# Optimization experiments

Hardware: AMD Instinct MI355X
Metric: run time of the kernel (lower is better)

The kernel has to match this reference:

```python
import jax, jax.numpy as jnp
import numpy as np

B, T, V, E, H = 16, 64, 32000, 256, 1024
NEG = -1e9


def lstm_step(kernel, bias, x, h, c):
    # TF BasicLSTMCell: gates ordered i, j, f, o; forget_bias = 1.0
    z = jnp.concatenate([x, h], axis=-1) @ kernel + bias
    i, j, f, o = jnp.split(z, 4, axis=-1)
    c_new = c * jax.nn.sigmoid(f + 1.0) + jax.nn.sigmoid(i) * jnp.tanh(j)
    h_new = jnp.tanh(c_new) * jax.nn.sigmoid(o)
    return h_new, c_new


def setup_inputs() -> dict:
    key = jax.random.key(0)
    ks = jax.random.split(key, 14)
    s = 0.05
    return {
        "encoder_inputs": jax.random.randint(ks[0], (B, T), 0, V, dtype=jnp.int32),
        "decoder_inputs": jax.random.randint(ks[1], (B, T), 0, V, dtype=jnp.int32),
        "encoder_lengths": jax.random.randint(ks[2], (B,), 1, T + 1, dtype=jnp.int32),
        "decoder_lengths": jax.random.randint(ks[3], (B,), 1, T + 1, dtype=jnp.int32),
        "embedding": jax.random.uniform(ks[4], (V, E), jnp.float32, -1 / 16, 1 / 16),
        "enc_kernel": jax.random.normal(ks[5], (E + H, 4 * H), jnp.float32) * s,
        "enc_bias": jnp.zeros((4 * H,), jnp.float32),
        "dec_kernel": jax.random.normal(ks[6], (E + H + H, 4 * H), jnp.float32) * s,
        "dec_bias": jnp.zeros((4 * H,), jnp.float32),
        "Wm": jax.random.normal(ks[7], (H, H), jnp.float32) * s,
        "Wq": jax.random.normal(ks[8], (H, H), jnp.float32) * s,
        "v_att": jax.random.normal(ks[9], (H,), jnp.float32) * s,
        "attn_kernel": jax.random.normal(ks[10], (2 * H, H), jnp.float32) * s,
        "out_kernel": jax.random.normal(ks[11], (H, V), jnp.float32) * s,
    }


def _forward(encoder_inputs, decoder_inputs, encoder_lengths, decoder_lengths,
             embedding, enc_kernel, enc_bias, dec_kernel, dec_bias,
             Wm, Wq, v_att, attn_kernel, out_kernel):
    q_emb = embedding[encoder_inputs]  # [B,T,E]
    r_emb = embedding[decoder_inputs]  # [B,T,E]

    # ---- encoder: dynamic_rnn with sequence_length semantics ----
    def enc_step(carry, inp):
        h, c = carry
        x, t = inp
        h2, c2 = lstm_step(enc_kernel, enc_bias, x, h, c)
        valid = (t < encoder_lengths)[:, None]
        h = jnp.where(valid, h2, h)
        c = jnp.where(valid, c2, c)
        out = jnp.where(valid, h2, 0.0)
        return (h, c), out

    h0 = jnp.zeros((B, H), jnp.float32)
    (enc_h, enc_c), memory_tm = jax.lax.scan(
        enc_step, (h0, h0), (q_emb.transpose(1, 0, 2), jnp.arange(T)))
    memory = memory_tm.transpose(1, 0, 2)  # [B,T,H]

    keys = memory @ Wm  # precomputed Bahdanau memory projection [B,T,H]
    score_mask = jnp.arange(T)[None, :] < encoder_lengths[:, None]  # [B,T]

    # ---- decoder: AttentionWrapper(BasicLSTMCell) + TrainingHelper ----
    def dec_step(carry, inp):
        h, c, attn = carry
        x_emb, t = inp
        x = jnp.concatenate([x_emb, attn], axis=-1)  # [B, E+H]
        h2, c2 = lstm_step(dec_kernel, dec_bias, x, h, c)
        query = h2 @ Wq  # [B,H]
        scores = jnp.einsum('bth,h->bt', jnp.tanh(keys + query[:, None, :]), v_att)
        scores = jnp.where(score_mask, scores, NEG)
        align = jax.nn.softmax(scores, axis=-1)  # [B,T]
        context = jnp.einsum('bt,bth->bh', align, memory)
        attn2 = jnp.concatenate([h2, context], axis=-1) @ attn_kernel  # [B,H]
        finished = (t >= decoder_lengths)[:, None]
        out = jnp.where(finished, 0.0, attn2)  # dynamic_decode zeros finished
        return (h2, c2, attn2), out

    attn0 = jnp.zeros((B, H), jnp.float32)
    _, dec_tm = jax.lax.scan(
        dec_step, (enc_h, enc_c, attn0), (r_emb.transpose(1, 0, 2), jnp.arange(T)))
    dec_out = dec_tm.transpose(1, 0, 2)  # [B,T,H]

    logits = jnp.einsum('bth,hv->btv', dec_out, out_kernel)  # [B,T,V]
    return logits


def reference(encoder_inputs, decoder_inputs, encoder_lengths, decoder_lengths,
              embedding, enc_kernel, enc_bias, dec_kernel, dec_bias,
              Wm, Wq, v_att, attn_kernel, out_kernel):
    return _forward(encoder_inputs, decoder_inputs, encoder_lengths, decoder_lengths,
                    embedding, enc_kernel, enc_bias, dec_kernel, dec_bias,
                    Wm, Wq, v_att, attn_kernel, out_kernel)
```

## Files before the change

### kernel.cpp

```cpp
#include <hip/hip_runtime.h>
#include <hip/hip_bf16.h>

#define B_ 16
#define T_ 64
#define V_ 32000
#define E_ 256
#define H_ 1024
#define G4_ (4 * H_)
#define KE_ (E_ + H_)
#define KD_ (E_ + 2*H_)
#define NKS_ 32
#define KSE_ (KE_ / NKS_)
#define KSD_ (KD_ / NKS_)

typedef unsigned short ushort_t;
typedef unsigned int uint_t;

__device__ __forceinline__ float b2f(ushort_t u) {
    return __uint_as_float(((uint_t)u) << 16);
}
__device__ __forceinline__ ushort_t f2b(float f) {
    uint_t u = __float_as_uint(f);
    u = (u + 0x7fffu + ((u >> 16) & 1u)) >> 16;
    return (ushort_t)u;
}
__device__ __forceinline__ float sigf(float x) {
    return 1.f / (1.f + expf(-x));
}

__global__ __launch_bounds__(256) void init_kernel(float* __restrict__ p, int n)
{
    int i = blockIdx.x * 256 + threadIdx.x;
    if (i < n) p[i] = 0.f;
}

__global__ __launch_bounds__(256) void enc_gemm_kernel(
    const float* __restrict__ emb, const int* __restrict__ enc_in,
    const float* __restrict__ Wk, const float* __restrict__ h_in,
    float* __restrict__ zpart, int t)
{
    const int cc = blockIdx.x & 15;
    const int ks = blockIdx.x >> 4;
    const int col = cc * 256 + threadIdx.x;
    const int k0 = ks * KSE_;

    int vidx[16];
    #pragma unroll
    for (int b = 0; b < 16; ++b) vidx[b] = enc_in[b * T_ + t];

    float acc[16];
    #pragma unroll
    for (int b = 0; b < 16; ++b) acc[b] = 0.f;

    for (int kk = 0; kk < KSE_; ++kk) {
        const int k = k0 + kk;
        const float w = Wk[(size_t)k * G4_ + col];
        if (k < E_) {
            #pragma unroll
            for (int b = 0; b < 16; ++b)
                acc[b] = fmaf(emb[(size_t)vidx[b] * E_ + k], w, acc[b]);
        } else {
            const float* hp = h_in + (k - E_);
            #pragma unroll
            for (int b = 0; b < 16; ++b)
                acc[b] = fmaf(hp[b * H_], w, acc[b]);
        }
    }
    #pragma unroll
    for (int b = 0; b < 16; ++b)
        zpart[((size_t)(ks * 16 + b)) * G4_ + col] = acc[b];
}

__global__ __launch_bounds__(256) void enc_gates_kernel(
    const float* __restrict__ zpart, const float* __restrict__ bias,
    const int* __restrict__ enc_len, const float* __restrict__ h_in,
    float* __restrict__ h_out, float* __restrict__ c,
    float* __restrict__ memory, int t)
{
    const int idx = blockIdx.x * 256 + threadIdx.x;
    const int b = idx >> 10, hu = idx & 1023;
    float z[4];
    #pragma unroll
    for (int g = 0; g < 4; ++g) {
        float s0 = bias[g * H_ + hu], s1 = 0.f, s2 = 0.f, s3 = 0.f;
        #pragma unroll
        for (int ks = 0; ks < NKS_; ks += 4) {
            s0 += zpart[((size_t)((ks + 0) * 16 + b)) * G4_ + g * H_ + hu];
            s1 += zpart[((size_t)((ks + 1) * 16 + b)) * G4_ + g * H_ + hu];
            s2 += zpart[((size_t)((ks + 2) * 16 + b)) * G4_ + g * H_ + hu];
            s3 += zpart[((size_t)((ks + 3) * 16 + b)) * G4_ + g * H_ + hu];
        }
        z[g] = (s0 + s1) + (s2 + s3);
    }
    const float cold = c[b * H_ + hu];
    const float cn = cold * sigf(z[2] + 1.f) + sigf(z[0]) * tanhf(z[1]);
    const float hn = tanhf(cn) * sigf(z[3]);
    const bool valid = t < enc_len[b];
    h_out[b * H_ + hu] = valid ? hn : h_in[b * H_ + hu];
    c[b * H_ + hu]     = valid ? cn : cold;
    memory[((size_t)b * T_ + t) * H_ + hu] = valid ? hn : 0.f;
}

__global__ __launch_bounds__(256) void keys_gemm_kernel(
    const float* __restrict__ memory, const float* __restrict__ Wm,
    float* __restrict__ keys)
{
    const int rt = blockIdx.x >> 2;
    const int cc = blockIdx.x & 3;
    const int col = cc * 256 + threadIdx.x;
    float acc[16];
    #pragma unroll
    for (int m = 0; m < 16; ++m) acc[m] = 0.f;
    for (int k = 0; k < H_; ++k) {
        const float w = Wm[(size_t)k * H_ + col];
        const float* mp = memory + (size_t)(rt * 16) * H_ + k;
        #pragma unroll
        for (int m = 0; m < 16; ++m)
            acc[m] = fmaf(mp[(size_t)m * H_], w, acc[m]);
    }
    #pragma unroll
    for (int m = 0; m < 16; ++m)
        keys[(size_t)(rt * 16 + m) * H_ + col] = acc[m];
}

__global__ __launch_bounds__(256) void dec_gemm_kernel(
    const float* __restrict__ emb, const int* __restrict__ dec_in,
    const float* __restrict__ Wk, const float* __restrict__ attn,
    const float* __restrict__ h_in, float* __restrict__ zpart, int t)
{
    const int cc = blockIdx.x & 15;
    const int ks = blockIdx.x >> 4;
    const int col = cc * 256 + threadIdx.x;
    const int k0 = ks * KSD_;

    int vidx[16];
    #pragma unroll
    for (int b = 0; b < 16; ++b) vidx[b] = dec_in[b * T_ + t];

    float acc[16];
    #pragma unroll
    for (int b = 0; b < 16; ++b) acc[b] = 0.f;

    for (int kk = 0; kk < KSD_; ++kk) {
        const int k = k0 + kk;
        const float w = Wk[(size_t)k * G4_ + col];
        if (k < E_) {
            #pragma unroll
            for (int b = 0; b < 16; ++b)
                acc[b] = fmaf(emb[(size_t)vidx[b] * E_ + k], w, acc[b]);
        } else if (k < E_ + H_) {
            const float* ap = attn + (k - E_);
            #pragma unroll
            for (int b = 0; b < 16; ++b)
                acc[b] = fmaf(ap[b * H_], w, acc[b]);
        } else {
            const float* hp = h_in + (k - E_ - H_);
            #pragma unroll
            for (int b = 0; b < 16; ++b)
                acc[b] = fmaf(hp[b * H_], w, acc[b]);
        }
    }
    #pragma unroll
    for (int b = 0; b < 16; ++b)
        zpart[((size_t)(ks * 16 + b)) * G4_ + col] = acc[b];
}

__global__ __launch_bounds__(256) void dec_gates_kernel(
    const float* __restrict__ zpart, const float* __restrict__ bias,
    float* __restrict__ h_out, float* __restrict__ c)
{
    const int idx = blockIdx.x * 256 + threadIdx.x;
    const int b = idx >> 10, hu = idx & 1023;
    float z[4];
    #pragma unroll
    for (int g = 0; g < 4; ++g) {
        float s0 = bias[g * H_ + hu], s1 = 0.f, s2 = 0.f, s3 = 0.f;
        #pragma unroll
        for (int ks = 0; ks < NKS_; ks += 4) {
            s0 += zpart[((size_t)((ks + 0) * 16 + b)) * G4_ + g * H_ + hu];
            s1 += zpart[((size_t)((ks + 1) * 16 + b)) * G4_ + g * H_ + hu];
            s2 += zpart[((size_t)((ks + 2) * 16 + b)) * G4_ + g * H_ + hu];
            s3 += zpart[((size_t)((ks + 3) * 16 + b)) * G4_ + g * H_ + hu];
        }
        z[g] = (s0 + s1) + (s2 + s3);
    }
    const float cold = c[b * H_ + hu];
    const float cn = cold * sigf(z[2] + 1.f) + sigf(z[0]) * tanhf(z[1]);
    const float hn = tanhf(cn) * sigf(z[3]);
    h_out[b * H_ + hu] = hn;
    c[b * H_ + hu] = cn;
}

__global__ __launch_bounds__(256) void query_gemm_kernel(
    const float* __restrict__ h2, const float* __restrict__ Wq,
    float* __restrict__ qpart)
{
    const int cc = blockIdx.x & 3;
    const int ks = blockIdx.x >> 2;
    const int col = cc * 256 + threadIdx.x;
    const int k0 = ks * 32;
    float acc[16];
    #pragma unroll
    for (int b = 0; b < 16; ++b) acc[b] = 0.f;
    for (int kk = 0; kk < 32; ++kk) {
        const int k = k0 + kk;
        const float w = Wq[(size_t)k * H_ + col];
        const float* hp = h2 + k;
        #pragma unroll
        for (int b = 0; b < 16; ++b)
            acc[b] = fmaf(hp[b * H_], w, acc[b]);
    }
    #pragma unroll
    for (int b = 0; b < 16; ++b)
        qpart[((size_t)(ks * 16 + b)) * H_ + col] = acc[b];
}

__global__ __launch_bounds__(256) void query_finish_kernel(
    const float* __restrict__ qpart, float* __restrict__ q)
{
    const int idx = blockIdx.x * 256 + threadIdx.x;
    const int b = idx >> 10, col = idx & 1023;
    float s0 = 0.f, s1 = 0.f, s2 = 0.f, s3 = 0.f;
    #pragma unroll
    for (int ks = 0; ks < 32; ks += 4) {
        s0 += qpart[((size_t)((ks + 0) * 16 + b)) * H_ + col];
        s1 += qpart[((size_t)((ks + 1) * 16 + b)) * H_ + col];
        s2 += qpart[((size_t)((ks + 2) * 16 + b)) * H_ + col];
        s3 += qpart[((size_t)((ks + 3) * 16 + b)) * H_ + col];
    }
    q[idx] = (s0 + s1) + (s2 + s3);
}

__global__ __launch_bounds__(256) void attn_scores_kernel(
    const float* __restrict__ q, const float* __restrict__ keys,
    const float* __restrict__ v_att, float* __restrict__ scores)
{
    const int b = blockIdx.x >> 6, t = blockIdx.x & 63;
    const int tid = threadIdx.x;
    const float* kp = keys + ((size_t)b * T_ + t) * H_;
    const float* qp = q + b * H_;
    float s = 0.f;
    #pragma unroll
    for (int i = 0; i < 4; ++i) {
        const int h = tid + i * 256;
        s += tanhf(kp[h] + qp[h]) * v_att[h];
    }
    #pragma unroll
    for (int off = 32; off; off >>= 1) s += __shfl_xor(s, off);
    __shared__ float red[4];
    if ((tid & 63) == 0) red[tid >> 6] = s;
    __syncthreads();
    if (tid == 0) scores[b * T_ + t] = (red[0] + red[1]) + (red[2] + red[3]);
}

__global__ __launch_bounds__(256) void softmax_ctx_kernel(
    const float* __restrict__ scores, const float* __restrict__ memory,
    const int* __restrict__ enc_len, float* __restrict__ ctx)
{
    const int b = blockIdx.x >> 2, cc = blockIdx.x & 3;
    const int tid = threadIdx.x;
    __shared__ float al[T_];
    if (tid < 64) {
        const int len = enc_len[b];
        float s = (tid < len) ? scores[b * T_ + tid] : -1e9f;
        float m = s;
        #pragma unroll
        for (int off = 32; off; off >>= 1) m = fmaxf(m, __shfl_xor(m, off));
        float e = expf(s - m);
        float sum = e;
        #pragma unroll
        for (int off = 32; off; off >>= 1) sum += __shfl_xor(sum, off);
        al[tid] = e / sum;
    }
    __syncthreads();
    const int col = cc * 256 + tid;
    const float* mp = memory + (size_t)b * T_ * H_ + col;
    float a0 = 0.f, a1 = 0.f, a2 = 0.f, a3 = 0.f;
    #pragma unroll
    for (int t2 = 0; t2 < T_; t2 += 4) {
        a0 = fmaf(al[t2 + 0], mp[(size_t)(t2 + 0) * H_], a0);
        a1 = fmaf(al[t2 + 1], mp[(size_t)(t2 + 1) * H_], a1);
        a2 = fmaf(al[t2 + 2], mp[(size_t)(t2 + 2) * H_], a2);
        a3 = fmaf(al[t2 + 3], mp[(size_t)(t2 + 3) * H_], a3);
    }
    ctx[b * H_ + col] = (a0 + a1) + (a2 + a3);
}

__global__ __launch_bounds__(256) void attnout_gemm_kernel(
    const float* __restrict__ h2, const float* __restrict__ ctx,
    const float* __restrict__ attn_k, float* __restrict__ apart)
{
    const int cc = blockIdx.x & 3;
    const int ks = blockIdx.x >> 2;
    const int col = cc * 256 + threadIdx.x;
    const int k0 = ks * 64;
    float acc[16];
    #pragma unroll
    for (int b = 0; b < 16; ++b) acc[b] = 0.f;
    for (int kk = 0; kk < 64; ++kk) {
        const int k = k0 + kk;
        const float w = attn_k[(size_t)k * H_ + col];
        const float* xp = (k < H_) ? (h2 + k) : (ctx + (k - H_));
        #pragma unroll
        for (int b = 0; b < 16; ++b)
            acc[b] = fmaf(xp[b * H_], w, acc[b]);
    }
    #pragma unroll
    for (int b = 0; b < 16; ++b)
        apart[((size_t)(ks * 16 + b)) * H_ + col] = acc[b];
}

__global__ __launch_bounds__(256) void attnout_finish_kernel(
    const float* __restrict__ apart, const int* __restrict__ dec_len,
    float* __restrict__ attn_state, float* __restrict__ dec_out, int t)
{
    const int idx = blockIdx.x * 256 + threadIdx.x;
    const int b = idx >> 10, col = idx & 1023;
    float s0 = 0.f, s1 = 0.f, s2 = 0.f, s3 = 0.f;
    #pragma unroll
    for (int ks = 0; ks < 32; ks += 4) {
        s0 += apart[((size_t)((ks + 0) * 16 + b)) * H_ + col];
        s1 += apart[((size_t)((ks + 1) * 16 + b)) * H_ + col];
        s2 += apart[((size_t)((ks + 2) * 16 + b)) * H_ + col];
        s3 += apart[((size_t)((ks + 3) * 16 + b)) * H_ + col];
    }
    const float s = (s0 + s1) + (s2 + s3);
    attn_state[b * H_ + col] = s;
    const bool fin = t >= dec_len[b];
    dec_out[((size_t)b * T_ + t) * H_ + col] = fin ? 0.f : s;
}

typedef __attribute__((ext_vector_type(8))) short short8;
typedef __attribute__((ext_vector_type(4))) float float4v;

__global__ __launch_bounds__(256) void logits_kernel(
    const float* __restrict__ A, const float* __restrict__ Bw,
    float* __restrict__ out)
{
    __shared__ __align__(16) ushort_t Ah[64][40];
    __shared__ __align__(16) ushort_t Al[64][40];
    __shared__ __align__(16) ushort_t Bh[64][40];
    __shared__ __align__(16) ushort_t Bl[64][40];
    const int tid = threadIdx.x;
    const int m0 = blockIdx.x * 64;
    const int n0 = blockIdx.y * 64;
    const int wv = tid >> 6, lane = tid & 63;
    const int ml = lane & 15, quad = lane >> 4;

    float4v acc[4];
    #pragma unroll
    for (int nn = 0; nn < 4; ++nn) acc[nn] = (float4v){0.f, 0.f, 0.f, 0.f};

    for (int kb = 0; kb < 1024; kb += 32) {
        __syncthreads();
        {
            const int r = tid >> 2, c0 = (tid & 3) * 8;
            const float* ap = A + (size_t)(m0 + r) * 1024 + kb + c0;
            #pragma unroll
            for (int i = 0; i < 8; ++i) {
                const float f = ap[i];
                const ushort_t hi = f2b(f);
                Ah[r][c0 + i] = hi;
                Al[r][c0 + i] = f2b(f - b2f(hi));
            }
        }
        {
            const int cB = tid & 63, kq = tid >> 6;
            #pragma unroll
            for (int i = 0; i < 8; ++i) {
                const int k = kq * 8 + i;
                const float f = Bw[(size_t)(kb + k) * V_ + n0 + cB];
                const ushort_t hi = f2b(f);
                Bh[cB][k] = hi;
                Bl[cB][k] = f2b(f - b2f(hi));
            }
        }
        __syncthreads();
        const short8 afh = *(const short8*)&Ah[wv * 16 + ml][quad * 8];
        const short8 afl = *(const short8*)&Al[wv * 16 + ml][quad * 8];
        #pragma unroll
        for (int nn = 0; nn < 4; ++nn) {
            const short8 bfh = *(const short8*)&Bh[nn * 16 + ml][quad * 8];
            const short8 bfl = *(const short8*)&Bl[nn * 16 + ml][quad * 8];
            acc[nn] = __builtin_amdgcn_mfma_f32_16x16x32_bf16(afh, bfh, acc[nn], 0, 0, 0);
            acc[nn] = __builtin_amdgcn_mfma_f32_16x16x32_bf16(afh, bfl, acc[nn], 0, 0, 0);
            acc[nn] = __builtin_amdgcn_mfma_f32_16x16x32_bf16(afl, bfh, acc[nn], 0, 0, 0);
        }
    }
    #pragma unroll
    for (int nn = 0; nn < 4; ++nn) {
        #pragma unroll
        for (int rg = 0; rg < 4; ++rg) {
            const int row = m0 + wv * 16 + quad * 4 + rg;
            const int colo = n0 + nn * 16 + ml;
            out[(size_t)row * V_ + colo] = acc[nn][rg];
        }
    }
}

extern "C" void kernel_launch(void* const* d_in, const int* in_sizes, int n_in,
                              void* d_out, int out_size, void* d_ws, size_t ws_size,
                              hipStream_t stream) {
    (void)in_sizes; (void)n_in; (void)out_size; (void)ws_size;
    const int*   enc_in  = (const int*)d_in[0];
    const int*   dec_in  = (const int*)d_in[1];
    const int*   enc_len = (const int*)d_in[2];
    const int*   dec_len = (const int*)d_in[3];
    const float* emb     = (const float*)d_in[4];
    const float* encK    = (const float*)d_in[5];
    const float* encB    = (const float*)d_in[6];
    const float* decK    = (const float*)d_in[7];
    const float* decB    = (const float*)d_in[8];
    const float* Wm      = (const float*)d_in[9];
    const float* Wq      = (const float*)d_in[10];
    const float* v_att   = (const float*)d_in[11];
    const float* attnK   = (const float*)d_in[12];
    const float* outK    = (const float*)d_in[13];
    float* out = (float*)d_out;

    float* hbuf    = (float*)d_ws;
    float* cbuf    = hbuf + 2 * B_ * H_;
    float* attn    = cbuf + B_ * H_;
    float* ctx     = attn + B_ * H_;
    float* q       = ctx + B_ * H_;
    float* scores  = q + B_ * H_;
    float* memory  = scores + B_ * T_;
    float* keys    = memory + (size_t)B_ * T_ * H_;
    float* dec_out = keys + (size_t)B_ * T_ * H_;
    float* zpart   = dec_out + (size_t)B_ * T_ * H_;
    float* qpart   = zpart;
    float* apart   = zpart + (size_t)32 * B_ * H_;

    const int ninit = 4 * B_ * H_;
    init_kernel<<<(ninit + 255) / 256, 256, 0, stream>>>((float*)d_ws, ninit);

    for (int t = 0; t < T_; ++t) {
        float* h_in  = hbuf + (t & 1) * B_ * H_;
        float* h_out = hbuf + ((t + 1) & 1) * B_ * H_;
        enc_gemm_kernel<<<512, 256, 0, stream>>>(emb, enc_in, encK, h_in, zpart, t);
        enc_gates_kernel<<<64, 256, 0, stream>>>(zpart, encB, enc_len, h_in,
                                                 h_out, cbuf, memory, t);
    }
    keys_gemm_kernel<<<256, 256, 0, stream>>>(memory, Wm, keys);

    for (int t = 0; t < T_; ++t) {
        float* h_in  = hbuf + (t & 1) * B_ * H_;
        float* h2    = hbuf + ((t + 1) & 1) * B_ * H_;
        dec_gemm_kernel<<<512, 256, 0, stream>>>(emb, dec_in, decK, attn, h_in, zpart, t);
        dec_gates_kernel<<<64, 256, 0, stream>>>(zpart, decB, h2, cbuf);
        query_gemm_kernel<<<128, 256, 0, stream>>>(h2, Wq, qpart);
        query_finish_kernel<<<64, 256, 0, stream>>>(qpart, q);
        attn_scores_kernel<<<1024, 256, 0, stream>>>(q, keys, v_att, scores);
        softmax_ctx_kernel<<<64, 256, 0, stream>>>(scores, memory, enc_len, ctx);
        attnout_gemm_kernel<<<128, 256, 0, stream>>>(h2, ctx, attnK, apart);
        attnout_finish_kernel<<<64, 256, 0, stream>>>(apart, dec_len, attn, dec_out, t);
    }

    logits_kernel<<<dim3(16, 500), 256, 0, stream>>>(dec_out, outK, out);
}
```

Before: 7.006 ms.

## Fuse per-step LSTM and attention kernels using atomic grid barriers

Merges each encoder and decoder step's GEMM and gate kernels into one launch. The partial sums are reduced by the last blocks after an atomic counter barrier. The six attention-stage kernels are collapsed into one persistent kernel of 256 blocks with five grid-wide barriers, and the inner loops load inputs as float4 with weights unrolled by four rows. This removes a large number of small kernel launches per timestep, but it depends on all blocks being co-resident and adds spin-wait and threadfence overhead.

```diff
diff --git a/kernel.cpp b/kernel.cpp
--- a/kernel.cpp
+++ b/kernel.cpp
@@ -1,5 +1,4 @@
 #include <hip/hip_runtime.h>
-#include <hip/hip_bf16.h>
 
 #define B_ 16
 #define T_ 64
@@ -28,20 +27,44 @@
     return 1.f / (1.f + expf(-x));
 }
 
-__global__ __launch_bounds__(256) void init_kernel(float* __restrict__ p, int n)
+__device__ __forceinline__ void block_arrive(int* cnt) {
+    __threadfence();
+    __syncthreads();
+    if (threadIdx.x == 0)
+        __hip_atomic_fetch_add(cnt, 1, __ATOMIC_RELEASE, __HIP_MEMORY_SCOPE_AGENT);
+}
+__device__ __forceinline__ void block_wait(int* cnt, int target) {
+    if (threadIdx.x == 0) {
+        while (__hip_atomic_load(cnt, __ATOMIC_ACQUIRE, __HIP_MEMORY_SCOPE_AGENT) < target)
+            __builtin_amdgcn_s_sleep(2);
+    }
+    __syncthreads();
+}
+__device__ __forceinline__ void grid_barrier(int* cnt, int target) {
+    block_arrive(cnt);
+    block_wait(cnt, target);
+}
+
+__global__ __launch_bounds__(256) void init_kernel(float* __restrict__ state,
+                                                   int* __restrict__ cnts)
 {
-    int i = blockIdx.x * 256 + threadIdx.x;
-    if (i < n) p[i] = 0.f;
-}
-
-__global__ __launch_bounds__(256) void enc_gemm_kernel(
+    const int i = blockIdx.x * 256 + threadIdx.x;
+    if (i < 4 * B_ * H_) state[i] = 0.f;
+    if (i < 256) cnts[i] = 0;
+}
+
+__global__ __launch_bounds__(256, 2) void enc_step_kernel(
     const float* __restrict__ emb, const int* __restrict__ enc_in,
-    const float* __restrict__ Wk, const float* __restrict__ h_in,
-    float* __restrict__ zpart, int t)
+    const float* __restrict__ Wk, const float* __restrict__ bias,
+    const int* __restrict__ enc_len, const float* __restrict__ h_in,
+    float* __restrict__ h_out, float* __restrict__ c,
+    float* __restrict__ memory, float* __restrict__ zpart,
+    int* __restrict__ cnt, int t)
 {
+    const int tid = threadIdx.x;
     const int cc = blockIdx.x & 15;
     const int ks = blockIdx.x >> 4;
-    const int col = cc * 256 + threadIdx.x;
+    const int col = cc * 256 + tid;
     const int k0 = ks * KSE_;
 
     int vidx[16];
@@ -52,43 +75,55 @@
     #pragma unroll
     for (int b = 0; b < 16; ++b) acc[b] = 0.f;
 
-    for (int kk = 0; kk < KSE_; ++kk) {
-        const int k = k0 + kk;
-        const float w = Wk[(size_t)k * G4_ + col];
+    for (int g = 0; g < KSE_ / 4; ++g) {
+        const int k = k0 + g * 4;
+        const float* wp = Wk + (size_t)k * G4_ + col;
+        const float w0 = wp[0];
+        const float w1 = wp[G4_];
+        const float w2 = wp[2 * G4_];
+        const float w3 = wp[3 * G4_];
         if (k < E_) {
             #pragma unroll
-            for (int b = 0; b < 16; ++b)
-                acc[b] = fmaf(emb[(size_t)vidx[b] * E_ + k], w, acc[b]);
+            for (int b = 0; b < 16; ++b) {
+                const float4 xv = *(const float4*)(emb + (size_t)vidx[b] * E_ + k);
+                acc[b] = fmaf(xv.x, w0, acc[b]);
+                acc[b] = fmaf(xv.y, w1, acc[b]);
+                acc[b] = fmaf(xv.z, w2, acc[b]);
+                acc[b] = fmaf(xv.w, w3, acc[b]);
+            }
         } else {
             const float* hp = h_in + (k - E_);
             #pragma unroll
-            for (int b = 0; b < 16; ++b)
-                acc[b] = fmaf(hp[b * H_], w, acc[b]);
+            for (int b = 0; b < 16; ++b) {
+                const float4 xv = *(const float4*)(hp + b * H_);
+                acc[b] = fmaf(xv.x, w0, acc[b]);
+                acc[b] = fmaf(xv.y, w1, acc[b]);
+                acc[b] = fmaf(xv.z, w2, acc[b]);
+                acc[b] = fmaf(xv.w, w3, acc[b]);
+            }
         }
     }
     #pragma unroll
     for (int b = 0; b < 16; ++b)
-        zpart[((size_t)(ks * 16 + b)) * G4_ + col] = acc[b];
-}
-
-__global__ __launch_bounds__(256) void enc_gates_kernel(
-    const float* __restrict__ zpart, const float* __restrict__ bias,
-    const int* __restrict__ enc_len, const float* __restrict__ h_in,
-    float* __restrict__ h_out, float* __restrict__ c,
-    float* __restrict__ memory, int t)
-{
-    const int idx = blockIdx.x * 256 + threadIdx.x;
+        zpart[(size_t)(ks * 16 + b) * G4_ + col] = acc[b];
+
+    block_arrive(cnt);
+    if (ks < 28) return;
+    block_wait(cnt, 512);
+
+    const int tb = (ks - 28) * 16 + cc;
+    const int idx = tb * 256 + tid;
     const int b = idx >> 10, hu = idx & 1023;
     float z[4];
     #pragma unroll
     for (int g = 0; g < 4; ++g) {
         float s0 = bias[g * H_ + hu], s1 = 0.f, s2 = 0.f, s3 = 0.f;
         #pragma unroll
-        for (int ks = 0; ks < NKS_; ks += 4) {
-            s0 += zpart[((size_t)((ks + 0) * 16 + b)) * G4_ + g * H_ + hu];
-            s1 += zpart[((size_t)((ks + 1) * 16 + b)) * G4_ + g * H_ + hu];
-            s2 += zpart[((size_t)((ks + 2) * 16 + b)) * G4_ + g * H_ + hu];
-            s3 += zpart[((size_t)((ks + 3) * 16 + b)) * G4_ + g * H_ + hu];
+        for (int kss = 0; kss < NKS_; kss += 4) {
+            s0 += zpart[(size_t)((kss + 0) * 16 + b) * G4_ + g * H_ + hu];
+            s1 += zpart[(size_t)((kss + 1) * 16 + b) * G4_ + g * H_ + hu];
+            s2 += zpart[(size_t)((kss + 2) * 16 + b) * G4_ + g * H_ + hu];
+            s3 += zpart[(size_t)((kss + 3) * 16 + b) * G4_ + g * H_ + hu];
         }
         z[g] = (s0 + s1) + (s2 + s3);
     }
@@ -111,26 +146,36 @@
     float acc[16];
     #pragma unroll
     for (int m = 0; m < 16; ++m) acc[m] = 0.f;
-    for (int k = 0; k < H_; ++k) {
-        const float w = Wm[(size_t)k * H_ + col];
+    for (int g = 0; g < H_ / 4; ++g) {
+        const int k = g * 4;
+        const float* wp = Wm + (size_t)k * H_ + col;
+        const float w0 = wp[0], w1 = wp[H_], w2 = wp[2 * H_], w3 = wp[3 * H_];
         const float* mp = memory + (size_t)(rt * 16) * H_ + k;
         #pragma unroll
-        for (int m = 0; m < 16; ++m)
-            acc[m] = fmaf(mp[(size_t)m * H_], w, acc[m]);
+        for (int m = 0; m < 16; ++m) {
+            const float4 xv = *(const float4*)(mp + (size_t)m * H_);
+            acc[m] = fmaf(xv.x, w0, acc[m]);
+            acc[m] = fmaf(xv.y, w1, acc[m]);
+            acc[m] = fmaf(xv.z, w2, acc[m]);
+            acc[m] = fmaf(xv.w, w3, acc[m]);
+        }
     }
     #pragma unroll
     for (int m = 0; m < 16; ++m)
         keys[(size_t)(rt * 16 + m) * H_ + col] = acc[m];
 }
 
-__global__ __launch_bounds__(256) void dec_gemm_kernel(
+__global__ __launch_bounds__(256, 2) void dec_step_kernel(
     const float* __restrict__ emb, const int* __restrict__ dec_in,
-    const float* __restrict__ Wk, const float* __restrict__ attn,
-    const float* __restrict__ h_in, float* __restrict__ zpart, int t)
+    const float* __restrict__ Wk, const float* __restrict__ bias,
+    const float* __restrict__ attn, const float* __restrict__ h_in,
+    float* __restrict__ h_out, float* __restrict__ c,
+    float* __restrict__ zpart, int* __restrict__ cnt, int t)
 {
+    const int tid = threadIdx.x;
     const int cc = blockIdx.x & 15;
     const int ks = blockIdx.x >> 4;
-    const int col = cc * 256 + threadIdx.x;
+    const int col = cc * 256 + tid;
     const int k0 = ks * KSD_;
 
     int vidx[16];
@@ -141,46 +186,56 @@
     #pragma unroll
     for (int b = 0; b < 16; ++b) acc[b] = 0.f;
 
-    for (int kk = 0; kk < KSD_; ++kk) {
-        const int k = k0 + kk;
-        const float w = Wk[(size_t)k * G4_ + col];
+    for (int g = 0; g < KSD_ / 4; ++g) {
+        const int k = k0 + g * 4;
+        const float* wp = Wk + (size_t)k * G4_ + col;
+        const float w0 = wp[0];
+        const float w1 = wp[G4_];
+        const float w2 = wp[2 * G4_];
+        const float w3 = wp[3 * G4_];
         if (k < E_) {
             #pragma unroll
-            for (int b = 0; b < 16; ++b)
-                acc[b] = fmaf(emb[(size_t)vidx[b] * E_ + k], w, acc[b]);
-        } else if (k < E_ + H_) {
-            const float* ap = attn + (k - E_);
-            #pragma unroll
-            for (int b = 0; b < 16; ++b)
-                acc[b] = fmaf(ap[b * H_], w, acc[b]);
+            for (int b = 0; b < 16; ++b) {
+                const float4 xv = *(const float4*)(emb + (size_t)vidx[b] * E_ + k);
+                acc[b] = fmaf(xv.x, w0, acc[b]);
+                acc[b] = fmaf(xv.y, w1, acc[b]);
+                acc[b] = fmaf(xv.z, w2, acc[b]);
+                acc[b] = fmaf(xv.w, w3, acc[b]);
+            }
         } else {
-            const float* hp = h_in + (k - E_ - H_);
-            #pragma unroll
-            for (int b = 0; b < 16; ++b)
-                acc[b] = fmaf(hp[b * H_], w, acc[b]);
+            const float* xb = (k < E_ + H_) ? (attn + (k - E_))
+                                            : (h_in + (k - E_ - H_));
+            #pragma unroll
+            for (int b = 0; b < 16; ++b) {
+                const float4 xv = *(const float4*)(xb + b * H_);
+                acc[b] = fmaf(xv.x, w0, acc[b]);
+                acc[b] = fmaf(xv.y, w1, acc[b]);
+                acc[b] = fmaf(xv.z, w2, acc[b]);
+                acc[b] = fmaf(xv.w, w3, acc[b]);
+            }
         }
     }
     #pragma unroll
     for (int b = 0; b < 16; ++b)
-        zpart[((size_t)(ks * 16 + b)) * G4_ + col] = acc[b];
-}
-
-__global__ __launch_bounds__(256) void dec_gates_kernel(
-    const float* __restrict__ zpart, const float* __restrict__ bias,
-    float* __restrict__ h_out, float* __restrict__ c)
-{
-    const int idx = blockIdx.x * 256 + threadIdx.x;
+        zpart[(size_t)(ks * 16 + b) * G4_ + col] = acc[b];
+
+    block_arrive(cnt);
+    if (ks < 28) return;
+    block_wait(cnt, 512);
+
+    const int tb = (ks - 28) * 16 + cc;
+    const int idx = tb * 256 + tid;
     const int b = idx >> 10, hu = idx & 1023;
     float z[4];
     #pragma unroll
     for (int g = 0; g < 4; ++g) {
         float s0 = bias[g * H_ + hu], s1 = 0.f, s2 = 0.f, s3 = 0.f;
         #pragma unroll
-        for (int ks = 0; ks < NKS_; ks += 4) {
-            s0 += zpart[((size_t)((ks + 0) * 16 + b)) * G4_ + g * H_ + hu];
-            s1 += zpart[((size_t)((ks + 1) * 16 + b)) * G4_ + g * H_ + hu];
-            s2 += zpart[((size_t)((ks + 2) * 16 + b)) * G4_ + g * H_ + hu];
-            s3 += zpart[((size_t)((ks + 3) * 16 + b)) * G4_ + g * H_ + hu];
+        for (int kss = 0; kss < NKS_; kss += 4) {
+            s0 += zpart[(size_t)((kss + 0) * 16 + b) * G4_ + g * H_ + hu];
+            s1 += zpart[(size_t)((kss + 1) * 16 + b) * G4_ + g * H_ + hu];
+            s2 += zpart[(size_t)((kss + 2) * 16 + b) * G4_ + g * H_ + hu];
+            s3 += zpart[(size_t)((kss + 3) * 16 + b) * G4_ + g * H_ + hu];
         }
         z[g] = (s0 + s1) + (s2 + s3);
     }
@@ -191,143 +246,156 @@
     c[b * H_ + hu] = cn;
 }
 
-__global__ __launch_bounds__(256) void query_gemm_kernel(
+__global__ __launch_bounds__(256, 2) void attn_mega_kernel(
     const float* __restrict__ h2, const float* __restrict__ Wq,
-    float* __restrict__ qpart)
+    float* __restrict__ qpart, float* __restrict__ q,
+    const float* __restrict__ keys, const float* __restrict__ v_att,
+    float* __restrict__ scores, const float* __restrict__ memory,
+    const int* __restrict__ enc_len, float* __restrict__ ctx,
+    const float* __restrict__ attnK, float* __restrict__ apart,
+    const int* __restrict__ dec_len, float* __restrict__ attn_state,
+    float* __restrict__ dec_out, int* __restrict__ cnt, int t)
 {
-    const int cc = blockIdx.x & 3;
-    const int ks = blockIdx.x >> 2;
-    const int col = cc * 256 + threadIdx.x;
-    const int k0 = ks * 32;
-    float acc[16];
-    #pragma unroll
-    for (int b = 0; b < 16; ++b) acc[b] = 0.f;
-    for (int kk = 0; kk < 32; ++kk) {
-        const int k = k0 + kk;
-        const float w = Wq[(size_t)k * H_ + col];
-        const float* hp = h2 + k;
+    const int tid = threadIdx.x;
+    const int blk = blockIdx.x;
+    __shared__ float al[T_];
+    __shared__ float red[4];
+
+    {
+        const int cc = blk & 3, ks = blk >> 2;
+        const int col = cc * 256 + tid;
+        const int k0 = ks * 16;
+        float acc[16];
+        #pragma unroll
+        for (int b = 0; b < 16; ++b) acc[b] = 0.f;
+        #pragma unroll
+        for (int g = 0; g < 4; ++g) {
+            const int k = k0 + g * 4;
+            const float* wp = Wq + (size_t)k * H_ + col;
+            const float w0 = wp[0], w1 = wp[H_], w2 = wp[2 * H_], w3 = wp[3 * H_];
+            #pragma unroll
+            for (int b = 0; b < 16; ++b) {
+                const float4 xv = *(const float4*)(h2 + b * H_ + k);
+                acc[b] = fmaf(xv.x, w0, acc[b]);
+                acc[b] = fmaf(xv.y, w1, acc[b]);
+                acc[b] = fmaf(xv.z, w2, acc[b]);
+                acc[b] = fmaf(xv.w, w3, acc[b]);
+            }
+        }
         #pragma unroll
         for (int b = 0; b < 16; ++b)
-            acc[b] = fmaf(hp[b * H_], w, acc[b]);
-    }
-    #pragma unroll
-    for (int b = 0; b < 16; ++b)
-        qpart[((size_t)(ks * 16 + b)) * H_ + col] = acc[b];
-}
-
-__global__ __launch_bounds__(256) void query_finish_kernel(
-    const float* __restrict__ qpart, float* __restrict__ q)
-{
-    const int idx = blockIdx.x * 256 + threadIdx.x;
-    const int b = idx >> 10, col = idx & 1023;
-    float s0 = 0.f, s1 = 0.f, s2 = 0.f, s3 = 0.f;
-    #pragma unroll
-    for (int ks = 0; ks < 32; ks += 4) {
-        s0 += qpart[((size_t)((ks + 0) * 16 + b)) * H_ + col];
-        s1 += qpart[((size_t)((ks + 1) * 16 + b)) * H_ + col];
-        s2 += qpart[((size_t)((ks + 2) * 16 + b)) * H_ + col];
-        s3 += qpart[((size_t)((ks + 3) * 16 + b)) * H_ + col];
-    }
-    q[idx] = (s0 + s1) + (s2 + s3);
-}
-
-__global__ __launch_bounds__(256) void attn_scores_kernel(
-    const float* __restrict__ q, const float* __restrict__ keys,
-    const float* __restrict__ v_att, float* __restrict__ scores)
-{
-    const int b = blockIdx.x >> 6, t = blockIdx.x & 63;
-    const int tid = threadIdx.x;
-    const float* kp = keys + ((size_t)b * T_ + t) * H_;
-    const float* qp = q + b * H_;
-    float s = 0.f;
+            qpart[(size_t)(ks * 16 + b) * H_ + col] = acc[b];
+    }
+    grid_barrier(cnt, 256);
+
+    if (blk < 64) {
+        const int idx = blk * 256 + tid;
+        const int b = idx >> 10, col = idx & 1023;
+        float s0 = 0.f, s1 = 0.f, s2 = 0.f, s3 = 0.f;
+        #pragma unroll
+        for (int ks = 0; ks < 64; ks += 4) {
+            s0 += qpart[(size_t)((ks + 0) * 16 + b) * H_ + col];
+            s1 += qpart[(size_t)((ks + 1) * 16 + b) * H_ + col];
+            s2 += qpart[(size_t)((ks + 2) * 16 + b) * H_ + col];
+            s3 += qpart[(size_t)((ks + 3) * 16 + b) * H_ + col];
+        }
+        q[idx] = (s0 + s1) + (s2 + s3);
+    }
+    grid_barrier(cnt, 512);
+
     #pragma unroll
     for (int i = 0; i < 4; ++i) {
-        const int h = tid + i * 256;
-        s += tanhf(kp[h] + qp[h]) * v_att[h];
-    }
-    #pragma unroll
-    for (int off = 32; off; off >>= 1) s += __shfl_xor(s, off);
-    __shared__ float red[4];
-    if ((tid & 63) == 0) red[tid >> 6] = s;
-    __syncthreads();
-    if (tid == 0) scores[b * T_ + t] = (red[0] + red[1]) + (red[2] + red[3]);
-}
-
-__global__ __launch_bounds__(256) void softmax_ctx_kernel(
-    const float* __restrict__ scores, const float* __restrict__ memory,
-    const int* __restrict__ enc_len, float* __restrict__ ctx)
-{
-    const int b = blockIdx.x >> 2, cc = blockIdx.x & 3;
-    const int tid = threadIdx.x;
-    __shared__ float al[T_];
-    if (tid < 64) {
-        const int len = enc_len[b];
-        float s = (tid < len) ? scores[b * T_ + tid] : -1e9f;
-        float m = s;
-        #pragma unroll
-        for (int off = 32; off; off >>= 1) m = fmaxf(m, __shfl_xor(m, off));
-        float e = expf(s - m);
-        float sum = e;
-        #pragma unroll
-        for (int off = 32; off; off >>= 1) sum += __shfl_xor(sum, off);
-        al[tid] = e / sum;
-    }
-    __syncthreads();
-    const int col = cc * 256 + tid;
-    const float* mp = memory + (size_t)b * T_ * H_ + col;
-    float a0 = 0.f, a1 = 0.f, a2 = 0.f, a3 = 0.f;
-    #pragma unroll
-    for (int t2 = 0; t2 < T_; t2 += 4) {
-        a0 = fmaf(al[t2 + 0], mp[(size_t)(t2 + 0) * H_], a0);
-        a1 = fmaf(al[t2 + 1], mp[(size_t)(t2 + 1) * H_], a1);
-        a2 = fmaf(al[t2 + 2], mp[(size_t)(t2 + 2) * H_], a2);
-        a3 = fmaf(al[t2 + 3], mp[(size_t)(t2 + 3) * H_], a3);
-    }
-    ctx[b * H_ + col] = (a0 + a1) + (a2 + a3);
-}
-
-__global__ __launch_bounds__(256) void attnout_gemm_kernel(
-    const float* __restrict__ h2, const float* __restrict__ ctx,
-    const float* __restrict__ attn_k, float* __restrict__ apart)
-{
-    const int cc = blockIdx.x & 3;
-    const int ks = blockIdx.x >> 2;
-    const int col = cc * 256 + threadIdx.x;
-    const int k0 = ks * 64;
-    float acc[16];
-    #pragma unroll
-    for (int b = 0; b < 16; ++b) acc[b] = 0.f;
-    for (int kk = 0; kk < 64; ++kk) {
-        const int k = k0 + kk;
-        const float w = attn_k[(size_t)k * H_ + col];
-        const float* xp = (k < H_) ? (h2 + k) : (ctx + (k - H_));
+        const int task = blk * 4 + i;
+        const int b = task >> 6, tt = task & 63;
+        const float* kp = keys + ((size_t)b * T_ + tt) * H_;
+        const float* qp = q + b * H_;
+        float s = 0.f;
+        #pragma unroll
+        for (int j = 0; j < 4; ++j) {
+            const int h = tid + j * 256;
+            s += tanhf(kp[h] + qp[h]) * v_att[h];
+        }
+        #pragma unroll
+        for (int off = 32; off; off >>= 1) s += __shfl_xor(s, off);
+        if ((tid & 63) == 0) red[tid >> 6] = s;
+        __syncthreads();
+        if (tid == 0) scores[b * T_ + tt] = (red[0] + red[1]) + (red[2] + red[3]);
+        __syncthreads();
+    }
+    grid_barrier(cnt, 768);
+
+    if (blk < 64) {
+        const int b = blk >> 2, cc = blk & 3;
+        if (tid < 64) {
+            const int len = enc_len[b];
+            float s = (tid < len) ? scores[b * T_ + tid] : -1e9f;
+            float m = s;
+            #pragma unroll
+            for (int off = 32; off; off >>= 1) m = fmaxf(m, __shfl_xor(m, off));
+            const float e = expf(s - m);
+            float sum = e;
+            #pragma unroll
+            for (int off = 32; off; off >>= 1) sum += __shfl_xor(sum, off);
+            al[tid] = e / sum;
+        }
+        __syncthreads();
+        const int col = cc * 256 + tid;
+        const float* mp = memory + (size_t)b * T_ * H_ + col;
+        float a0 = 0.f, a1 = 0.f, a2 = 0.f, a3 = 0.f;
+        #pragma unroll
+        for (int t2 = 0; t2 < T_; t2 += 4) {
+            a0 = fmaf(al[t2 + 0], mp[(size_t)(t2 + 0) * H_], a0);
+            a1 = fmaf(al[t2 + 1], mp[(size_t)(t2 + 1) * H_], a1);
+            a2 = fmaf(al[t2 + 2], mp[(size_t)(t2 + 2) * H_], a2);
+            a3 = fmaf(al[t2 + 3], mp[(size_t)(t2 + 3) * H_], a3);
+        }
+        ctx[b * H_ + col] = (a0 + a1) + (a2 + a3);
+    }
+    grid_barrier(cnt, 1024);
+
+    {
+        const int cc = blk & 3, ks = blk >> 2;
+        const int col = cc * 256 + tid;
+        const int k0 = ks * 32;
+        float acc[16];
+        #pragma unroll
+        for (int b = 0; b < 16; ++b) acc[b] = 0.f;
+        #pragma unroll
+        for (int g = 0; g < 8; ++g) {
+            const int k = k0 + g * 4;
+            const float* wp = attnK + (size_t)k * H_ + col;
+            const float w0 = wp[0], w1 = wp[H_], w2 = wp[2 * H_], w3 = wp[3 * H_];
+            const float* xb = (k < H_) ? (h2 + k) : (ctx + (k - H_));
+            #pragma unroll
+            for (int b = 0; b < 16; ++b) {
+                const float4 xv = *(const float4*)(xb + b * H_);
+                acc[b] = fmaf(xv.x, w0, acc[b]);
+                acc[b] = fmaf(xv.y, w1, acc[b]);
+                acc[b] = fmaf(xv.z, w2, acc[b]);
+                acc[b] = fmaf(xv.w, w3, acc[b]);
+            }
+        }
         #pragma unroll
         for (int b = 0; b < 16; ++b)
-            acc[b] = fmaf(xp[b * H_], w, acc[b]);
-    }
-    #pragma unroll
-    for (int b = 0; b < 16; ++b)
-        apart[((size_t)(ks * 16 + b)) * H_ + col] = acc[b];
-}
-
-__global__ __launch_bounds__(256) void attnout_finish_kernel(
-    const float* __restrict__ apart, const int* __restrict__ dec_len,
-    float* __restrict__ attn_state, float* __restrict__ dec_out, int t)
-{
-    const int idx = blockIdx.x * 256 + threadIdx.x;
-    const int b = idx >> 10, col = idx & 1023;
-    float s0 = 0.f, s1 = 0.f, s2 = 0.f, s3 = 0.f;
-    #pragma unroll
-    for (int ks = 0; ks < 32; ks += 4) {
-        s0 += apart[((size_t)((ks + 0) * 16 + b)) * H_ + col];
-        s1 += apart[((size_t)((ks + 1) * 16 + b)) * H_ + col];
-        s2 += apart[((size_t)((ks + 2) * 16 + b)) * H_ + col];
-        s3 += apart[((size_t)((ks + 3) * 16 + b)) * H_ + col];
-    }
-    const float s = (s0 + s1) + (s2 + s3);
-    attn_state[b * H_ + col] = s;
-    const bool fin = t >= dec_len[b];
-    dec_out[((size_t)b * T_ + t) * H_ + col] = fin ? 0.f : s;
+            apart[(size_t)(ks * 16 + b) * H_ + col] = acc[b];
+    }
+    grid_barrier(cnt, 1280);
+
+    if (blk < 64) {
+        const int idx = blk * 256 + tid;
+        const int b = idx >> 10, col = idx & 1023;
+        float s0 = 0.f, s1 = 0.f, s2 = 0.f, s3 = 0.f;
+        #pragma unroll
+        for (int ks = 0; ks < 64; ks += 4) {
+            s0 += apart[(size_t)((ks + 0) * 16 + b) * H_ + col];
+            s1 += apart[(size_t)((ks + 1) * 16 + b) * H_ + col];
+            s2 += apart[(size_t)((ks + 2) * 16 + b) * H_ + col];
+            s3 += apart[(size_t)((ks + 3) * 16 + b) * H_ + col];
+        }
+        const float s = (s0 + s1) + (s2 + s3);
+        attn_state[b * H_ + col] = s;
+        dec_out[((size_t)b * T_ + t) * H_ + col] = (t >= dec_len[b]) ? 0.f : s;
+    }
 }
 
 typedef __attribute__((ext_vector_type(8))) short short8;
@@ -429,31 +497,30 @@
     float* dec_out = keys + (size_t)B_ * T_ * H_;
     float* zpart   = dec_out + (size_t)B_ * T_ * H_;
     float* qpart   = zpart;
-    float* apart   = zpart + (size_t)32 * B_ * H_;
-
-    const int ninit = 4 * B_ * H_;
-    init_kernel<<<(ninit + 255) / 256, 256, 0, stream>>>((float*)d_ws, ninit);
+    float* apart   = zpart + (size_t)64 * B_ * H_;
+    int*   cnts    = (int*)(zpart + (size_t)NKS_ * B_ * G4_);
+
+    init_kernel<<<256, 256, 0, stream>>>((float*)d_ws, cnts);
 
     for (int t = 0; t < T_; ++t) {
         float* h_in  = hbuf + (t & 1) * B_ * H_;
         float* h_out = hbuf + ((t + 1) & 1) * B_ * H_;
-        enc_gemm_kernel<<<512, 256, 0, stream>>>(emb, enc_in, encK, h_in, zpart, t);
-        enc_gates_kernel<<<64, 256, 0, stream>>>(zpart, encB, enc_len, h_in,
-                                                 h_out, cbuf, memory, t);
+        enc_step_kernel<<<512, 256, 0, stream>>>(emb, enc_in, encK, encB, enc_len,
+                                                 h_in, h_out, cbuf, memory, zpart,
+                                                 cnts + t, t);
     }
     keys_gemm_kernel<<<256, 256, 0, stream>>>(memory, Wm, keys);
 
     for (int t = 0; t < T_; ++t) {
-        float* h_in  = hbuf + (t & 1) * B_ * H_;
-        float* h2    = hbuf + ((t + 1) & 1) * B_ * H_;
-        dec_gemm_kernel<<<512, 256, 0, stream>>>(emb, dec_in, decK, attn, h_in, zpart, t);
-        dec_gates_kernel<<<64, 256, 0, stream>>>(zpart, decB, h2, cbuf);
-        query_gemm_kernel<<<128, 256, 0, stream>>>(h2, Wq, qpart);
-        query_finish_kernel<<<64, 256, 0, stream>>>(qpart, q);
-        attn_scores_kernel<<<1024, 256, 0, stream>>>(q, keys, v_att, scores);
-        softmax_ctx_kernel<<<64, 256, 0, stream>>>(scores, memory, enc_len, ctx);
-        attnout_gemm_kernel<<<128, 256, 0, stream>>>(h2, ctx, attnK, apart);
-        attnout_finish_kernel<<<64, 256, 0, stream>>>(apart, dec_len, attn, dec_out, t);
+        float* h_in = hbuf + (t & 1) * B_ * H_;
+        float* h2   = hbuf + ((t + 1) & 1) * B_ * H_;
+        dec_step_kernel<<<512, 256, 0, stream>>>(emb, dec_in, decK, decB, attn,
+                                                 h_in, h2, cbuf, zpart,
+                                                 cnts + 64 + t, t);
+        attn_mega_kernel<<<256, 256, 0, stream>>>(h2, Wq, qpart, q, keys, v_att,
+                                                  scores, memory, enc_len, ctx,
+                                                  attnK, apart, dec_len, attn,
+                                                  dec_out, cnts + 128 + t, t);
     }
 
     logits_kernel<<<dim3(16, 500), 256, 0, stream>>>(dec_out, outK, out);
```

Result: slower. 26.57 ms (+279.2%).
